# Optimization experiments

Hardware: AMD Instinct MI355X
Metric: run time of the kernel (lower is better)

The kernel has to match this reference:

```python
import jax, jax.numpy as jnp
import numpy as np

B, NPG, H, D = 8, 6250, 4, 128   # graphs, nodes/graph, heads, hidden
N = B * NPG                       # 50000 nodes total
E = 400000                        # edges
VOCAB = 10000


def setup_inputs() -> dict:
    key = jax.random.key(0)
    ks = jax.random.split(key, 12)
    p = lambda k, shape: jax.random.normal(k, shape, dtype=jnp.float32) * 0.05
    return {
        "node_ids": jax.random.randint(ks[0], (N,), 0, VOCAB),
        "src": jax.random.randint(ks[1], (E,), 0, N),
        "dst": jax.random.randint(ks[2], (E,), 0, N),
        "emb": p(ks[3], (VOCAB, D)),
        "W_src": p(ks[4], (D, H * D)), "b_src": jnp.zeros((H * D,), jnp.float32),
        "W_dst": p(ks[5], (D, H * D)), "b_dst": jnp.zeros((H * D,), jnp.float32),
        "attn": p(ks[6], (H, D)),
        "W_res": p(ks[7], (D, H * D)), "b_res": jnp.zeros((H * D,), jnp.float32),
        "W_gc": p(ks[8], (D, D)), "b_gc": jnp.zeros((D,), jnp.float32),
        "W_mlp": p(ks[9], (3 * D, 1)), "b_mlp": jnp.zeros((1,), jnp.float32),
    }


def _leaky(x, s):
    return jnp.where(x >= 0, x, s * x)


def _maxpool(feat):
    # dgl.max_nodes: per-graph max over nodes -> [B, feat_dim]
    return jnp.max(feat.reshape(B, NPG, -1), axis=1)


def _gatv2(x, src, dst, W_src, b_src, W_dst, b_dst, attn, W_res, b_res):
    # DGL GATv2Conv (share_weights=False, residual=True, eval mode -> no dropout)
    hs = (x @ W_src + b_src).reshape(N, H, D)
    hd = (x @ W_dst + b_dst).reshape(N, H, D)
    e = _leaky(hs[src] + hd[dst], 0.2)              # [E,H,D]
    logits = jnp.einsum('ehd,hd->eh', e, attn)      # [E,H]
    m = jax.ops.segment_max(logits, dst, num_segments=N)
    ex = jnp.exp(logits - m[dst])
    denom = jax.ops.segment_sum(ex, dst, num_segments=N)
    alpha = ex / denom[dst]                          # edge softmax per dst/head
    rst = jax.ops.segment_sum(hs[src] * alpha[..., None], dst, num_segments=N)
    rst = rst + (x @ W_res + b_res).reshape(N, H, D)
    return _leaky(rst, 0.01)                         # nn.LeakyReLU() activation


def _graphconv(x, src, dst, W, b):
    # DGL GraphConv norm='both', allow_zero_in_degree=True, LeakyReLU activation
    ones = jnp.ones((E,), x.dtype)
    dout = jnp.clip(jax.ops.segment_sum(ones, src, num_segments=N), 1.0, None)
    din = jnp.clip(jax.ops.segment_sum(ones, dst, num_segments=N), 1.0, None)
    h = x * jax.lax.rsqrt(dout)[:, None]
    agg = jax.ops.segment_sum(h[src], dst, num_segments=N)
    h = agg * jax.lax.rsqrt(din)[:, None]
    return _leaky(h @ W + b, 0.01)


def reference(node_ids, src, dst, emb, W_src, b_src, W_dst, b_dst, attn,
              W_res, b_res, W_gc, b_gc, W_mlp, b_mlp):
    feat = emb[node_ids]                             # featurize_nodes
    pools = [_maxpool(feat)]
    res = _gatv2(feat, src, dst, W_src, b_src, W_dst, b_dst, attn,
                 W_res, b_res).mean(axis=1)          # mean over heads -> [N,D]
    pools.append(_maxpool(res))
    res = _graphconv(res, src, dst, W_gc, b_gc)
    pools.append(_maxpool(res))
    agg = jnp.concatenate(pools, axis=1)             # [B, 3D]
    # reward_predictor_block_two: ReLU -> (Dropout eval) -> Linear(3D, 1)
    return jax.nn.relu(agg) @ W_mlp + b_mlp          # BCE logits [B,1]
```

## Files before the change

### kernel.cpp

```cpp
#include <hip/hip_runtime.h>
#include <float.h>
#include <math.h>

#define Bg   8
#define NPGc 6250
#define Hh   4
#define Dd   128
#define Nn   50000
#define Ee   400000
#define HDd  512
#define WNf  1536
#define NCHUNK 49

typedef unsigned short ushort_t;
typedef __attribute__((ext_vector_type(8))) short bf16x8;
typedef __attribute__((ext_vector_type(4))) float f32x4;

__device__ __forceinline__ void atomicMaxF(float* addr, float val) {
    if (val >= 0.0f) atomicMax((int*)addr, __float_as_int(val));
    else             atomicMin((unsigned int*)addr, __float_as_uint(val));
}

__device__ __forceinline__ ushort_t f2bf(float x) {
    unsigned u = __float_as_uint(x);
    unsigned r = (u + 0x7FFFu + ((u >> 16) & 1u)) >> 16;
    return (ushort_t)r;
}

__device__ __forceinline__ void bf2x2(unsigned u, float& lo, float& hi) {
    lo = __uint_as_float(u << 16);
    hi = __uint_as_float(u & 0xFFFF0000u);
}

__device__ __forceinline__ void gload16(const void* g, void* l) {
    __builtin_amdgcn_global_load_lds(
        (const __attribute__((address_space(1))) unsigned int*)g,
        (__attribute__((address_space(3))) unsigned int*)l, 16, 0, 0);
}

__global__ void init_kernel(int* din_i, float* dout, int* cursor, float* pools) {
    int i = blockIdx.x * blockDim.x + threadIdx.x;
    if (i < Nn) { din_i[i] = 0; dout[i] = 0.0f; cursor[i] = 0; }
    if (i < Bg * 3 * Dd) pools[i] = -FLT_MAX;
}

__global__ void gather_kernel(const int* __restrict__ ids, const float* __restrict__ emb,
                              float* __restrict__ feat, ushort_t* __restrict__ feat_bf) {
    int i = blockIdx.x * blockDim.x + threadIdx.x;
    int n = i >> 5, c = i & 31;
    int id = ids[n];
    float4 v = ((const float4*)emb)[(size_t)id * 32 + c];
    ((float4*)feat)[(size_t)n * 32 + c] = v;
    ushort4 b;
    b.x = f2bf(v.x); b.y = f2bf(v.y); b.z = f2bf(v.z); b.w = f2bf(v.w);
    ((ushort4*)feat_bf)[(size_t)n * 32 + c] = b;
}

__global__ void maxpool_kernel(const float* __restrict__ x, float* __restrict__ pools, int col_off) {
    int b = blockIdx.x, chunk = blockIdx.y, d = threadIdx.x;
    int i0 = chunk * 125, i1 = i0 + 125;
    float mx = -FLT_MAX;
    for (int i = i0; i < i1; ++i)
        mx = fmaxf(mx, x[((size_t)(b * NPGc + i)) * Dd + d]);
    atomicMaxF(&pools[b * (3 * Dd) + col_off + d], mx);
}

__global__ void prep_kernel(const float* __restrict__ W_src, const float* __restrict__ W_dst,
                            const float* __restrict__ W_res, const float* __restrict__ W_gc,
                            const float* __restrict__ b_src, const float* __restrict__ b_dst,
                            const float* __restrict__ b_res,
                            ushort_t* __restrict__ Wt, ushort_t* __restrict__ Wt_gc,
                            float* __restrict__ bias_f) {
    int i = blockIdx.x * blockDim.x + threadIdx.x;
    if (i < WNf * 128) {
        int c = i >> 7, k = i & 127;
        float v = (c < 512) ? W_src[k * 512 + c]
                : (c < 1024) ? W_dst[k * 512 + (c - 512)]
                             : W_res[k * 512 + (c - 1024)];
        Wt[i] = f2bf(v);
    } else if (i < WNf * 128 + 128 * 128) {
        int j = i - WNf * 128;
        int c = j >> 7, k = j & 127;
        Wt_gc[j] = f2bf(W_gc[k * 128 + c]);
    }
    if (i < WNf)
        bias_f[i] = (i < 512) ? b_src[i] : (i < 1024) ? b_dst[i - 512] : b_res[i - 1024];
}

__global__ __launch_bounds__(256) void mfma_gemm_kernel(
    const ushort_t* __restrict__ A, const ushort_t* __restrict__ Wt,
    const float* __restrict__ bias, ushort_t* __restrict__ Ob, float* __restrict__ Of,
    int n_rows, int WN, int do_leak)
{
    __shared__ char Ws[2][16384] __attribute__((aligned(16)));
    int row0 = blockIdx.x * 64;
    int tid = threadIdx.x;
    int w = tid >> 6, lane = tid & 63;
    int lrow = lane & 15, kg = lane >> 4;
    int NC = WN >> 6;

    bf16x8 av[4][4];
    {
        const ushort_t* ap = A + (size_t)(row0 + lrow) * 128 + kg * 8;
        #pragma unroll
        for (int fi = 0; fi < 4; ++fi)
            #pragma unroll
            for (int ks = 0; ks < 4; ++ks)
                av[fi][ks] = *(const bf16x8*)(ap + (size_t)fi * 16 * 128 + ks * 32);
    }

    auto stage = [&](int ct, int buf) {
        #pragma unroll
        for (int i = 0; i < 4; ++i) {
            int s = i * 4096 + w * 1024 + lane * 16;
            int r = s >> 8;
            int p = (s >> 4) & 15;
            int sbyte = (p * 16) ^ ((r & 7) << 4);
            const ushort_t* g = Wt + (size_t)(ct * 64 + r) * 128 + (sbyte >> 1);
            gload16(g, &Ws[buf][i * 4096 + w * 1024]);
        }
    };

    stage(0, 0);
    __syncthreads();

    for (int ct = 0; ct < NC; ++ct) {
        int cur = ct & 1;
        if (ct + 1 < NC) stage(ct + 1, cur ^ 1);

        bf16x8 wv[4];
        {
            const char* lb = Ws[cur] + (w * 16 + lrow) * 256;
            #pragma unroll
            for (int ks = 0; ks < 4; ++ks) {
                int byte = (kg * 16 + ks * 64) ^ ((lrow & 7) << 4);
                wv[ks] = *(const bf16x8*)(lb + byte);
            }
        }

        f32x4 acc[4] = {};
        #pragma unroll
        for (int ks = 0; ks < 4; ++ks)
            #pragma unroll
            for (int fi = 0; fi < 4; ++fi)
                acc[fi] = __builtin_amdgcn_mfma_f32_16x16x32_bf16(wv[ks], av[fi][ks], acc[fi], 0, 0, 0);

        int colb = ct * 64 + w * 16 + kg * 4;
        float4 bv4 = *(const float4*)(bias + colb);
        #pragma unroll
        for (int fi = 0; fi < 4; ++fi) {
            int grow = row0 + fi * 16 + lrow;
            if (grow < n_rows) {
                float o[4];
                #pragma unroll
                for (int j = 0; j < 4; ++j) {
                    float v = acc[fi][j] + ((const float*)&bv4)[j];
                    if (do_leak) v = v >= 0.0f ? v : 0.01f * v;
                    o[j] = v;
                }
                if (Ob) {
                    ushort4 ob;
                    ob.x = f2bf(o[0]); ob.y = f2bf(o[1]); ob.z = f2bf(o[2]); ob.w = f2bf(o[3]);
                    *(ushort4*)(Ob + (size_t)grow * WN + colb) = ob;
                } else {
                    *(float4*)(Of + (size_t)grow * WN + colb) = *(float4*)o;
                }
            }
        }
        __syncthreads();
    }
}

__global__ void degree2_kernel(const int* __restrict__ src, const int* __restrict__ dst,
                               int* __restrict__ din_i, float* __restrict__ dout) {
    int e = blockIdx.x * blockDim.x + threadIdx.x;
    if (e >= Ee) return;
    atomicAdd(&din_i[dst[e]], 1);
    atomicAdd(&dout[src[e]], 1.0f);
}

__global__ __launch_bounds__(256) void scan_reduce_kernel(const int* __restrict__ din_i,
                                                          int* __restrict__ partials) {
    int b = blockIdx.x, t = threadIdx.x;
    int base = b * 1024 + t * 4;
    int s = 0;
    #pragma unroll
    for (int j = 0; j < 4; ++j) { int i = base + j; if (i < Nn) s += din_i[i]; }
    #pragma unroll
    for (int off = 32; off > 0; off >>= 1) s += __shfl_xor(s, off);
    __shared__ int wsum[4];
    if ((t & 63) == 0) wsum[t >> 6] = s;
    __syncthreads();
    if (t == 0) partials[b] = wsum[0] + wsum[1] + wsum[2] + wsum[3];
}

__global__ void scan_mid_kernel(int* __restrict__ partials, int* __restrict__ row_start) {
    if (threadIdx.x == 0) {
        int acc = 0;
        for (int i = 0; i < NCHUNK; ++i) { int v = partials[i]; partials[i] = acc; acc += v; }
        row_start[Nn] = acc;
    }
}

__global__ __launch_bounds__(256) void scan_final_kernel(const int* __restrict__ din_i,
                                                         const int* __restrict__ partials,
                                                         int* __restrict__ row_start,
                                                         float* __restrict__ din_f) {
    int b = blockIdx.x, t = threadIdx.x;
    int base = b * 1024 + t * 4;
    int v[4]; int s = 0;
    #pragma unroll
    for (int j = 0; j < 4; ++j) {
        v[j] = (base + j < Nn) ? din_i[base + j] : 0;
        s += v[j];
    }
    __shared__ int buf[256];
    buf[t] = s;
    __syncthreads();
    #pragma unroll
    for (int off = 1; off < 256; off <<= 1) {
        int x = (t >= off) ? buf[t - off] : 0;
        __syncthreads();
        buf[t] += x;
        __syncthreads();
    }
    int excl = buf[t] - s + partials[b];
    #pragma unroll
    for (int j = 0; j < 4; ++j) {
        if (base + j < Nn) {
            row_start[base + j] = excl;
            din_f[base + j] = (float)v[j];
            excl += v[j];
        }
    }
}

__global__ void scatter_kernel(const int* __restrict__ src, const int* __restrict__ dst,
                               const int* __restrict__ row_start, int* __restrict__ cursor,
                               int* __restrict__ csr_src) {
    int e = blockIdx.x * blockDim.x + threadIdx.x;
    if (e >= Ee) return;
    int d = dst[e];
    int slot = row_start[d] + atomicAdd(&cursor[d], 1);
    csr_src[slot] = src[e];
}

__global__ __launch_bounds__(256) void gat_fused_kernel(
    const ushort_t* __restrict__ h_all, const float* __restrict__ attn,
    const int* __restrict__ row_start, const int* __restrict__ csr_src,
    float* __restrict__ res)
{
    int d = (blockIdx.x * 256 + threadIdx.x) >> 6;
    int lane = threadIdx.x & 63;
    if (d >= Nn) return;
    int e0 = row_start[d], e1 = row_start[d + 1];

    float hdv[8], atv[8];
    {
        uint4 hr = *(const uint4*)(h_all + (size_t)d * WNf + 512 + lane * 8);
        bf2x2(hr.x, hdv[0], hdv[1]); bf2x2(hr.y, hdv[2], hdv[3]);
        bf2x2(hr.z, hdv[4], hdv[5]); bf2x2(hr.w, hdv[6], hdv[7]);
        float4 a0 = *(const float4*)(attn + lane * 8);
        float4 a1 = *(const float4*)(attn + lane * 8 + 4);
        atv[0] = a0.x; atv[1] = a0.y; atv[2] = a0.z; atv[3] = a0.w;
        atv[4] = a1.x; atv[5] = a1.y; atv[6] = a1.z; atv[7] = a1.w;
    }

    float m = -FLT_MAX, denom = 0.0f;
    float acc[8] = {};

    int s = (e0 < e1) ? csr_src[e0] : 0;
    for (int e = e0; e < e1; ++e) {
        int s_next = (e + 1 < e1) ? csr_src[e + 1] : 0;
        uint4 raw = *(const uint4*)(h_all + (size_t)s * WNf + lane * 8);
        float hsv[8];
        bf2x2(raw.x, hsv[0], hsv[1]); bf2x2(raw.y, hsv[2], hsv[3]);
        bf2x2(raw.z, hsv[4], hsv[5]); bf2x2(raw.w, hsv[6], hsv[7]);
        float p = 0.0f;
        #pragma unroll
        for (int j = 0; j < 8; ++j) {
            float x = hsv[j] + hdv[j];
            x = x >= 0.0f ? x : 0.2f * x;
            p = fmaf(x, atv[j], p);
        }
        p += __shfl_xor(p, 1); p += __shfl_xor(p, 2);
        p += __shfl_xor(p, 4); p += __shfl_xor(p, 8);
        float mn = fmaxf(m, p);
        float corr = expf(m - mn);
        float ex = expf(p - mn);
        denom = denom * corr + ex;
        #pragma unroll
        for (int j = 0; j < 8; ++j) acc[j] = fmaf(acc[j], corr, hsv[j] * ex);
        m = mn;
        s = s_next;
    }

    float inv = (e1 > e0) ? 1.0f / denom : 0.0f;
    float rv[8];
    {
        uint4 rr = *(const uint4*)(h_all + (size_t)d * WNf + 1024 + lane * 8);
        bf2x2(rr.x, rv[0], rv[1]); bf2x2(rr.y, rv[2], rv[3]);
        bf2x2(rr.z, rv[4], rv[5]); bf2x2(rr.w, rv[6], rv[7]);
    }
    float t[8];
    #pragma unroll
    for (int j = 0; j < 8; ++j) {
        float v = fmaf(acc[j], inv, rv[j]);
        t[j] = v >= 0.0f ? v : 0.01f * v;
    }
    #pragma unroll
    for (int j = 0; j < 8; ++j) {
        t[j] += __shfl_xor(t[j], 16);
        t[j] += __shfl_xor(t[j], 32);
    }
    if (lane < 16) {
        float o0[4] = {0.25f * t[0], 0.25f * t[1], 0.25f * t[2], 0.25f * t[3]};
        float o1[4] = {0.25f * t[4], 0.25f * t[5], 0.25f * t[6], 0.25f * t[7]};
        *(float4*)(res + (size_t)d * Dd + lane * 8)     = *(float4*)o0;
        *(float4*)(res + (size_t)d * Dd + lane * 8 + 4) = *(float4*)o1;
    }
}

__global__ __launch_bounds__(256) void gc_gather_kernel(
    const float* __restrict__ res, const int* __restrict__ row_start,
    const int* __restrict__ csr_src, const float* __restrict__ dout,
    const float* __restrict__ din, ushort_t* __restrict__ agg_bf)
{
    int d = (blockIdx.x * 256 + threadIdx.x) >> 6;
    int lane = threadIdx.x & 63;
    if (d >= Nn) return;
    int e0 = row_start[d], e1 = row_start[d + 1];
    float ax = 0.0f, ay = 0.0f;
    int s = (e0 < e1) ? csr_src[e0] : 0;
    for (int e = e0; e < e1; ++e) {
        int s_next = (e + 1 < e1) ? csr_src[e + 1] : 0;
        float sc = 1.0f / sqrtf(fmaxf(dout[s], 1.0f));
        float2 v = ((const float2*)(res + (size_t)s * Dd))[lane];
        ax = fmaf(v.x, sc, ax);
        ay = fmaf(v.y, sc, ay);
        s = s_next;
    }
    float scd = 1.0f / sqrtf(fmaxf(din[d], 1.0f));
    ushort2 o;
    o.x = f2bf(ax * scd);
    o.y = f2bf(ay * scd);
    ((ushort2*)(agg_bf + (size_t)d * Dd))[lane] = o;
}

__global__ void final_kernel(const float* __restrict__ pools, const float* __restrict__ W_mlp,
                             const float* __restrict__ b_mlp, float* __restrict__ out) {
    int b = blockIdx.x, lane = threadIdx.x;
    float s = 0.0f;
    for (int j = lane; j < 3 * Dd; j += 64)
        s += fmaxf(pools[b * (3 * Dd) + j], 0.0f) * W_mlp[j];
    #pragma unroll
    for (int off = 32; off > 0; off >>= 1) s += __shfl_xor(s, off);
    if (lane == 0) out[b] = s + b_mlp[0];
}

extern "C" void kernel_launch(void* const* d_in, const int* in_sizes, int n_in,
                              void* d_out, int out_size, void* d_ws, size_t ws_size,
                              hipStream_t stream) {
    const int*   node_ids = (const int*)d_in[0];
    const int*   src      = (const int*)d_in[1];
    const int*   dst      = (const int*)d_in[2];
    const float* emb      = (const float*)d_in[3];
    const float* W_src    = (const float*)d_in[4];
    const float* b_src    = (const float*)d_in[5];
    const float* W_dst    = (const float*)d_in[6];
    const float* b_dst    = (const float*)d_in[7];
    const float* attn     = (const float*)d_in[8];
    const float* W_res    = (const float*)d_in[9];
    const float* b_res    = (const float*)d_in[10];
    const float* W_gc     = (const float*)d_in[11];
    const float* b_gc     = (const float*)d_in[12];
    const float* W_mlp    = (const float*)d_in[13];
    const float* b_mlp    = (const float*)d_in[14];
    float* out = (float*)d_out;

    char* w = (char*)d_ws;
    size_t off = 0;
    float*    feat    = (float*)(w + off);    off += (size_t)Nn * Dd * 4;
    ushort_t* feat_bf = (ushort_t*)(w + off); off += (size_t)(Nn + 64) * Dd * 2;
    ushort_t* h_all   = (ushort_t*)(w + off); off += (size_t)Nn * WNf * 2;
    ushort_t* Wt      = (ushort_t*)(w + off); off += (size_t)WNf * 128 * 2;
    ushort_t* Wt_gc   = (ushort_t*)(w + off); off += (size_t)128 * 128 * 2;
    float*    bias_f  = (float*)(w + off);    off += (size_t)WNf * 4;
    int*      csr_src = (int*)(w + off);      off += (size_t)Ee * 4;
    int*      row_st  = (int*)(w + off);      off += ((size_t)Nn + 4) * 4;
    int*      cursor  = (int*)(w + off);      off += (size_t)Nn * 4;
    int*      din_i   = (int*)(w + off);      off += (size_t)Nn * 4;
    float*    din_f   = (float*)(w + off);    off += (size_t)Nn * 4;
    float*    dout_f  = (float*)(w + off);    off += (size_t)Nn * 4;
    int*      partials= (int*)(w + off);      off += 64 * 4;
    float*    pools   = (float*)(w + off);    off += (size_t)Bg * 3 * Dd * 4;

    float*    res    = feat;
    ushort_t* agg_bf = h_all;
    float*    res2   = (float*)(w + (size_t)Nn * Dd * 6 + (size_t)(Nn + 64) * Dd * 2);

    init_kernel<<<(Nn + 255) / 256, 256, 0, stream>>>(din_i, dout_f, cursor, pools);
    gather_kernel<<<(Nn * 32) / 256, 256, 0, stream>>>(node_ids, emb, feat, feat_bf);
    maxpool_kernel<<<dim3(Bg, 50), Dd, 0, stream>>>(feat, pools, 0);

    prep_kernel<<<(WNf * 128 + 128 * 128 + 255) / 256, 256, 0, stream>>>(
        W_src, W_dst, W_res, W_gc, b_src, b_dst, b_res, Wt, Wt_gc, bias_f);

    degree2_kernel<<<(Ee + 255) / 256, 256, 0, stream>>>(src, dst, din_i, dout_f);
    scan_reduce_kernel<<<NCHUNK, 256, 0, stream>>>(din_i, partials);
    scan_mid_kernel<<<1, 64, 0, stream>>>(partials, row_st);
    scan_final_kernel<<<NCHUNK, 256, 0, stream>>>(din_i, partials, row_st, din_f);
    scatter_kernel<<<(Ee + 255) / 256, 256, 0, stream>>>(src, dst, row_st, cursor, csr_src);

    mfma_gemm_kernel<<<(Nn + 63) / 64, 256, 0, stream>>>(
        feat_bf, Wt, bias_f, h_all, nullptr, Nn, WNf, 0);

    gat_fused_kernel<<<(Nn * 64) / 256, 256, 0, stream>>>(h_all, attn, row_st, csr_src, res);
    maxpool_kernel<<<dim3(Bg, 50), Dd, 0, stream>>>(res, pools, Dd);

    gc_gather_kernel<<<(Nn * 64) / 256, 256, 0, stream>>>(res, row_st, csr_src, dout_f, din_f, agg_bf);
    mfma_gemm_kernel<<<(Nn + 63) / 64, 256, 0, stream>>>(
        agg_bf, Wt_gc, b_gc, nullptr, res2, Nn, Dd, 1);
    maxpool_kernel<<<dim3(Bg, 50), Dd, 0, stream>>>(res2, pools, 2 * Dd);

    final_kernel<<<Bg, 64, 0, stream>>>(pools, W_mlp, b_mlp, out);
}
```

Before: 413.3 us.

## Load GEMM weights directly to registers, split columns across grid, prefetch gather rows

The MFMA GEMM no longer stages weight tiles through LDS with global_load_lds and barriers. Each wave now loads its weight fragments straight from global memory into registers, double-buffered across column tiles. The wide projection GEMM is split over two grid columns to raise block count. Separately, the GAT and GraphConv gather loops now prefetch the next source row's features (and degree scale) one edge ahead to hide gather latency. The cost is more register pressure and redundant global weight reads per wave instead of shared LDS reuse, and the two-tile loop assumes an even tile count per block.

New measurement: 403.7 us. 1.02x faster.

```diff
diff --git a/kernel.cpp b/kernel.cpp
--- a/kernel.cpp
+++ b/kernel.cpp
@@ -30,12 +30,6 @@
 __device__ __forceinline__ void bf2x2(unsigned u, float& lo, float& hi) {
     lo = __uint_as_float(u << 16);
     hi = __uint_as_float(u & 0xFFFF0000u);
-}
-
-__device__ __forceinline__ void gload16(const void* g, void* l) {
-    __builtin_amdgcn_global_load_lds(
-        (const __attribute__((address_space(1))) unsigned int*)g,
-        (__attribute__((address_space(3))) unsigned int*)l, 16, 0, 0);
 }
 
 __global__ void init_kernel(int* din_i, float* dout, int* cursor, float* pools) {
@@ -92,12 +86,12 @@
     const float* __restrict__ bias, ushort_t* __restrict__ Ob, float* __restrict__ Of,
     int n_rows, int WN, int do_leak)
 {
-    __shared__ char Ws[2][16384] __attribute__((aligned(16)));
-    int row0 = blockIdx.x * 64;
-    int tid = threadIdx.x;
-    int w = tid >> 6, lane = tid & 63;
+    int ncols = WN >> 6;
+    int ntile = ncols / gridDim.y;
+    int ct0   = blockIdx.y * ntile;
+    int row0  = blockIdx.x * 64;
+    int w = threadIdx.x >> 6, lane = threadIdx.x & 63;
     int lrow = lane & 15, kg = lane >> 4;
-    int NC = WN >> 6;
 
     bf16x8 av[4][4];
     {
@@ -106,46 +100,14 @@
         for (int fi = 0; fi < 4; ++fi)
             #pragma unroll
             for (int ks = 0; ks < 4; ++ks)
-                av[fi][ks] = *(const bf16x8*)(ap + (size_t)fi * 16 * 128 + ks * 32);
-    }
-
-    auto stage = [&](int ct, int buf) {
-        #pragma unroll
-        for (int i = 0; i < 4; ++i) {
-            int s = i * 4096 + w * 1024 + lane * 16;
-            int r = s >> 8;
-            int p = (s >> 4) & 15;
-            int sbyte = (p * 16) ^ ((r & 7) << 4);
-            const ushort_t* g = Wt + (size_t)(ct * 64 + r) * 128 + (sbyte >> 1);
-            gload16(g, &Ws[buf][i * 4096 + w * 1024]);
-        }
-    };
-
-    stage(0, 0);
-    __syncthreads();
-
-    for (int ct = 0; ct < NC; ++ct) {
-        int cur = ct & 1;
-        if (ct + 1 < NC) stage(ct + 1, cur ^ 1);
-
-        bf16x8 wv[4];
-        {
-            const char* lb = Ws[cur] + (w * 16 + lrow) * 256;
-            #pragma unroll
-            for (int ks = 0; ks < 4; ++ks) {
-                int byte = (kg * 16 + ks * 64) ^ ((lrow & 7) << 4);
-                wv[ks] = *(const bf16x8*)(lb + byte);
-            }
-        }
-
-        f32x4 acc[4] = {};
-        #pragma unroll
-        for (int ks = 0; ks < 4; ++ks)
-            #pragma unroll
-            for (int fi = 0; fi < 4; ++fi)
-                acc[fi] = __builtin_amdgcn_mfma_f32_16x16x32_bf16(wv[ks], av[fi][ks], acc[fi], 0, 0, 0);
-
-        int colb = ct * 64 + w * 16 + kg * 4;
+                av[fi][ks] = *(const bf16x8*)(ap + fi * 16 * 128 + ks * 32);
+    }
+
+    const ushort_t* wp = Wt + (size_t)(ct0 * 64 + w * 16 + lrow) * 128 + kg * 8;
+    const size_t TSTR = 64 * 128;
+
+    auto epi = [&](int ctt, f32x4 (&acc)[4]) {
+        int colb = (ct0 + ctt) * 64 + w * 16 + kg * 4;
         float4 bv4 = *(const float4*)(bias + colb);
         #pragma unroll
         for (int fi = 0; fi < 4; ++fi) {
@@ -167,7 +129,39 @@
                 }
             }
         }
-        __syncthreads();
+    };
+
+    bf16x8 wvA[4], wvB[4];
+    #pragma unroll
+    for (int ks = 0; ks < 4; ++ks) wvA[ks] = *(const bf16x8*)(wp + ks * 32);
+
+    for (int ct = 0; ct < ntile; ct += 2) {
+        #pragma unroll
+        for (int ks = 0; ks < 4; ++ks)
+            wvB[ks] = *(const bf16x8*)(wp + (size_t)(ct + 1) * TSTR + ks * 32);
+        {
+            f32x4 acc[4] = {};
+            #pragma unroll
+            for (int ks = 0; ks < 4; ++ks)
+                #pragma unroll
+                for (int fi = 0; fi < 4; ++fi)
+                    acc[fi] = __builtin_amdgcn_mfma_f32_16x16x32_bf16(wvA[ks], av[fi][ks], acc[fi], 0, 0, 0);
+            epi(ct, acc);
+        }
+        if (ct + 2 < ntile) {
+            #pragma unroll
+            for (int ks = 0; ks < 4; ++ks)
+                wvA[ks] = *(const bf16x8*)(wp + (size_t)(ct + 2) * TSTR + ks * 32);
+        }
+        {
+            f32x4 acc[4] = {};
+            #pragma unroll
+            for (int ks = 0; ks < 4; ++ks)
+                #pragma unroll
+                for (int fi = 0; fi < 4; ++fi)
+                    acc[fi] = __builtin_amdgcn_mfma_f32_16x16x32_bf16(wvB[ks], av[fi][ks], acc[fi], 0, 0, 0);
+            epi(ct + 1, acc);
+        }
     }
 }
 
@@ -270,9 +264,10 @@
     float acc[8] = {};
 
     int s = (e0 < e1) ? csr_src[e0] : 0;
+    uint4 raw = *(const uint4*)(h_all + (size_t)s * WNf + lane * 8);
     for (int e = e0; e < e1; ++e) {
-        int s_next = (e + 1 < e1) ? csr_src[e + 1] : 0;
-        uint4 raw = *(const uint4*)(h_all + (size_t)s * WNf + lane * 8);
+        int s_next = (e + 1 < e1) ? csr_src[e + 1] : s;
+        uint4 raw_next = *(const uint4*)(h_all + (size_t)s_next * WNf + lane * 8);
         float hsv[8];
         bf2x2(raw.x, hsv[0], hsv[1]); bf2x2(raw.y, hsv[2], hsv[3]);
         bf2x2(raw.z, hsv[4], hsv[5]); bf2x2(raw.w, hsv[6], hsv[7]);
@@ -292,7 +287,7 @@
         #pragma unroll
         for (int j = 0; j < 8; ++j) acc[j] = fmaf(acc[j], corr, hsv[j] * ex);
         m = mn;
-        s = s_next;
+        raw = raw_next;
     }
 
     float inv = (e1 > e0) ? 1.0f / denom : 0.0f;
@@ -332,13 +327,16 @@
     int e0 = row_start[d], e1 = row_start[d + 1];
     float ax = 0.0f, ay = 0.0f;
     int s = (e0 < e1) ? csr_src[e0] : 0;
+    float sc = 1.0f / sqrtf(fmaxf((e0 < e1) ? dout[s] : 1.0f, 1.0f));
+    float2 v = (e0 < e1) ? ((const float2*)(res + (size_t)s * Dd))[lane] : make_float2(0.f, 0.f);
     for (int e = e0; e < e1; ++e) {
-        int s_next = (e + 1 < e1) ? csr_src[e + 1] : 0;
-        float sc = 1.0f / sqrtf(fmaxf(dout[s], 1.0f));
-        float2 v = ((const float2*)(res + (size_t)s * Dd))[lane];
+        int s_next = (e + 1 < e1) ? csr_src[e + 1] : s;
+        float sc_n = 1.0f / sqrtf(fmaxf(dout[s_next], 1.0f));
+        float2 v_n = ((const float2*)(res + (size_t)s_next * Dd))[lane];
         ax = fmaf(v.x, sc, ax);
         ay = fmaf(v.y, sc, ay);
-        s = s_next;
+        sc = sc_n;
+        v = v_n;
     }
     float scd = 1.0f / sqrtf(fmaxf(din[d], 1.0f));
     ushort2 o;
@@ -412,14 +410,14 @@
     scan_final_kernel<<<NCHUNK, 256, 0, stream>>>(din_i, partials, row_st, din_f);
     scatter_kernel<<<(Ee + 255) / 256, 256, 0, stream>>>(src, dst, row_st, cursor, csr_src);
 
-    mfma_gemm_kernel<<<(Nn + 63) / 64, 256, 0, stream>>>(
+    mfma_gemm_kernel<<<dim3((Nn + 63) / 64, 2), 256, 0, stream>>>(
         feat_bf, Wt, bias_f, h_all, nullptr, Nn, WNf, 0);
 
     gat_fused_kernel<<<(Nn * 64) / 256, 256, 0, stream>>>(h_all, attn, row_st, csr_src, res);
     maxpool_kernel<<<dim3(Bg, 50), Dd, 0, stream>>>(res, pools, Dd);
 
     gc_gather_kernel<<<(Nn * 64) / 256, 256, 0, stream>>>(res, row_st, csr_src, dout_f, din_f, agg_bf);
-    mfma_gemm_kernel<<<(Nn + 63) / 64, 256, 0, stream>>>(
+    mfma_gemm_kernel<<<dim3((Nn + 63) / 64, 1), 256, 0, stream>>>(
         agg_bf, Wt_gc, b_gc, nullptr, res2, Nn, Dd, 1);
     maxpool_kernel<<<dim3(Bg, 50), Dd, 0, stream>>>(res2, pools, 2 * Dd);
 
```
